# Performance work log

Hardware: AMD Instinct MI355X
Metric: run time of the kernel (lower is better)

Reference implementation:

```python
import jax, jax.numpy as jnp
import numpy as np

N = 100000    # nodes
E = 1200000   # edges (avg degree 12)
D0, D1 = 512, 256         # modality input dims
H, L, DEC = 500, 128, 64  # encoder hidden, latent, decoder dims
F1, F2, C = 64, 64, 8     # gnn hidden feats, num classes
EPS = 1e-5


def _bn(x, g, b, m, v):
    # inference-mode BatchNorm1d with running stats
    return (x - m) * jax.lax.rsqrt(v + EPS) * g + b


def _encoder(x, W1, b1, g1, be1, m1, v1, W2, b2, g2, be2, m2, v2, Wd, bd):
    e = _bn(x @ W1.T + b1, g1, be1, m1, v1)   # [N, H]
    e = _bn(e @ W2.T + b2, g2, be2, m2, v2)   # [N, L]
    return e @ Wd.T + bd                      # decoded: [N, DEC]


def _sage_pool(h, src, dst, Wp, bp, Ws, Wn, b):
    # DGL SAGEConv aggregator_type='pool' (feat_drop is identity in eval):
    # h_neigh[v] = max_{u in N(v)} relu(fc_pool(h[u])); out = fc_self(h) + fc_neigh(h_neigh) + bias
    m = jax.nn.relu(h @ Wp.T + bp)                              # [N, Din]
    agg = jax.ops.segment_max(m[src], dst, num_segments=N)      # gather + max-scatter
    agg = jnp.where(jnp.isfinite(agg), agg, 0.0)                # isolated nodes -> 0 (DGL)
    return h @ Ws.T + agg @ Wn.T + b


def setup_inputs() -> dict:
    key = jax.random.key(0)
    ks = iter(jax.random.split(key, 80))

    def nrm(sh, s=0.02):
        return jax.random.normal(next(ks), sh, jnp.float32) * s

    inp = {}
    inp["x0"] = jax.random.normal(next(ks), (N, D0), jnp.float32)
    inp["x1"] = jax.random.normal(next(ks), (N, D1), jnp.float32)
    inp["src"] = jax.random.randint(next(ks), (E,), 0, N, jnp.int32)
    inp["dst"] = jax.random.randint(next(ks), (E,), 0, N, jnp.int32)
    for mi, d in enumerate((D0, D1)):
        p = f"enc{mi}_"
        inp[p + "W1"] = nrm((H, d)); inp[p + "b1"] = jnp.zeros((H,), jnp.float32)
        inp[p + "g1"] = jnp.ones((H,), jnp.float32); inp[p + "be1"] = jnp.zeros((H,), jnp.float32)
        inp[p + "m1"] = nrm((H,), 0.1)
        inp[p + "v1"] = jax.random.uniform(next(ks), (H,), jnp.float32, 0.5, 1.5)
        inp[p + "W2"] = nrm((L, H)); inp[p + "b2"] = jnp.zeros((L,), jnp.float32)
        inp[p + "g2"] = jnp.ones((L,), jnp.float32); inp[p + "be2"] = jnp.zeros((L,), jnp.float32)
        inp[p + "m2"] = nrm((L,), 0.1)
        inp[p + "v2"] = jax.random.uniform(next(ks), (L,), jnp.float32, 0.5, 1.5)
        inp[p + "Wd"] = nrm((DEC, L)); inp[p + "bd"] = jnp.zeros((DEC,), jnp.float32)
    for li, (i, o) in enumerate(((DEC, F1), (F1, F2), (F2, C))):
        p = f"s{li}_"
        inp[p + "Wp"] = nrm((i, i)); inp[p + "bp"] = jnp.zeros((i,), jnp.float32)
        inp[p + "Ws"] = nrm((o, i)); inp[p + "Wn"] = nrm((o, i))
        inp[p + "b"] = jnp.zeros((o,), jnp.float32)
    return inp


def reference(x0, x1, src, dst,
              enc0_W1, enc0_b1, enc0_g1, enc0_be1, enc0_m1, enc0_v1,
              enc0_W2, enc0_b2, enc0_g2, enc0_be2, enc0_m2, enc0_v2, enc0_Wd, enc0_bd,
              enc1_W1, enc1_b1, enc1_g1, enc1_be1, enc1_m1, enc1_v1,
              enc1_W2, enc1_b2, enc1_g2, enc1_be2, enc1_m2, enc1_v2, enc1_Wd, enc1_bd,
              s0_Wp, s0_bp, s0_Ws, s0_Wn, s0_b,
              s1_Wp, s1_bp, s1_Ws, s1_Wn, s1_b,
              s2_Wp, s2_bp, s2_Ws, s2_Wn, s2_b):
    d0 = _encoder(x0, enc0_W1, enc0_b1, enc0_g1, enc0_be1, enc0_m1, enc0_v1,
                  enc0_W2, enc0_b2, enc0_g2, enc0_be2, enc0_m2, enc0_v2, enc0_Wd, enc0_bd)
    d1 = _encoder(x1, enc1_W1, enc1_b1, enc1_g1, enc1_be1, enc1_m1, enc1_v1,
                  enc1_W2, enc1_b2, enc1_g2, enc1_be2, enc1_m2, enc1_v2, enc1_Wd, enc1_bd)
    # mean over modalities (dropout = identity in eval; imputation/reindex = identity with full coverage)
    feat = (d0 + d1) * 0.5
    h = jax.nn.relu(_sage_pool(feat, src, dst, s0_Wp, s0_bp, s0_Ws, s0_Wn, s0_b))
    h = jax.nn.relu(_sage_pool(h, src, dst, s1_Wp, s1_bp, s1_Ws, s1_Wn, s1_b))
    h = _sage_pool(h, src, dst, s2_Wp, s2_bp, s2_Ws, s2_Wn, s2_b)  # [N, C]
    return h
```

## Files before the change

### kernel.cpp

```cpp
#include <hip/hip_runtime.h>
#include <hip/hip_bf16.h>

#define EPSV 1e-5f
#define NBUCK_C 400
using u16 = unsigned short;
using u32 = unsigned int;
typedef __attribute__((ext_vector_type(8))) short short8;
typedef __attribute__((ext_vector_type(4))) float f32x4;

__device__ __forceinline__ u16 f2bf(float f) {
  __hip_bfloat16 h = __float2bfloat16(f);
  u16 u; __builtin_memcpy(&u, &h, 2); return u;
}

__device__ __forceinline__ void gload16(const void* g, void* l) {
  __builtin_amdgcn_global_load_lds(
      (const __attribute__((address_space(1))) void*)g,
      (__attribute__((address_space(3))) void*)l, 16, 0, 0);
}

__device__ __forceinline__ u32 mx2(u32 a, u32 b) {
  u32 ah = a & 0xFFFF0000u, bh = b & 0xFFFF0000u;
  u32 al = a & 0x0000FFFFu, bl = b & 0x0000FFFFu;
  return (ah > bh ? ah : bh) | (al > bl ? al : bl);
}
__device__ __forceinline__ uint4 mx4(uint4 a, uint4 b) {
  return make_uint4(mx2(a.x, b.x), mx2(a.y, b.y), mx2(a.z, b.z), mx2(a.w, b.w));
}

struct EncR { float4 a[4]; short8 b[2]; };

__global__ __launch_bounds__(256) void enc_fused64(
    const float* __restrict__ x0, const float* __restrict__ x1,
    const u16* __restrict__ W0, const u16* __restrict__ W1,
    const float* __restrict__ beff0, const float* __restrict__ beff1,
    const u16* __restrict__ Wp, const float* __restrict__ bp,
    u16* __restrict__ out, u16* __restrict__ mout, int M) {
  __shared__ u16 sA[64 * 64];
  __shared__ u16 sB[64 * 64];
  const int tid = threadIdx.x;
  const int l = tid & 63;
  const int w = tid >> 6;
  const int row0 = blockIdx.x * 64;
  const int lc = l & 15;
  const int koff = (l >> 4) * 8;

  f32x4 acc[4];
#pragma unroll
  for (int nf = 0; nf < 4; ++nf) acc[nf] = f32x4{0.f, 0.f, 0.f, 0.f};

  auto loadstep = [&](EncR& rs, int s) {
    const int ph = s >= 8;
    const float* X = ph ? x1 : x0;
    const u16* W = ph ? W1 : W0;
    const int lda = ph ? 256 : 512;
    const int kb = (s - (ph ? 8 : 0)) * 64;
#pragma unroll
    for (int c = 0; c < 2; ++c) {
      const int r = c * 32 + (tid >> 3);
      const int gr = min(row0 + r, M - 1);
      const float* gp = &X[(size_t)gr * lda + kb + ((tid & 7) << 3)];
      rs.a[c * 2] = *(const float4*)gp;
      rs.a[c * 2 + 1] = *(const float4*)(gp + 4);
    }
#pragma unroll
    for (int i = 0; i < 2; ++i) {
      const int s2 = tid * 2 + i;
      const int rb = s2 >> 3, sl = s2 & 7;
      rs.b[i] = *(const short8*)&W[rb * lda + kb + sl * 8];
    }
  };
  auto storestep = [&](const EncR& rs) {
#pragma unroll
    for (int c = 0; c < 2; ++c) {
      const int r = c * 32 + (tid >> 3);
      const int ssl = tid & 7;
      short8 pk;
#pragma unroll
      for (int j = 0; j < 4; ++j) pk[j] = (short)f2bf(rs.a[c * 2][j]);
#pragma unroll
      for (int j = 0; j < 4; ++j) pk[4 + j] = (short)f2bf(rs.a[c * 2 + 1][j]);
      *(short8*)&sA[r * 64 + ((ssl ^ (r & 7)) << 3)] = pk;
    }
#pragma unroll
    for (int i = 0; i < 2; ++i) {
      const int s2 = tid * 2 + i;
      const int rb = s2 >> 3, sl = s2 & 7;
      *(short8*)&sB[rb * 64 + ((sl ^ (rb & 7)) << 3)] = rs.b[i];
    }
  };
  auto compute = [&]() {
#pragma unroll
    for (int kk = 0; kk < 2; ++kk) {
      const int r = w * 16 + lc;
      const int sl = kk * 4 + (l >> 4);
      const short8 af = *(const short8*)&sA[r * 64 + ((sl ^ (r & 7)) << 3)];
#pragma unroll
      for (int nf = 0; nf < 4; ++nf) {
        const int rb = nf * 16 + lc;
        const short8 bf = *(const short8*)&sB[rb * 64 + ((sl ^ (rb & 7)) << 3)];
        acc[nf] = __builtin_amdgcn_mfma_f32_16x16x32_bf16(af, bf, acc[nf], 0, 0, 0);
      }
    }
  };

  EncR rA, rB;
  loadstep(rA, 0);
  for (int s = 0; s < 12; s += 2) {
    loadstep(rB, s + 1);
    storestep(rA);
    __syncthreads();
    compute();
    __syncthreads();
    if (s + 2 < 12) loadstep(rA, s + 2);
    storestep(rB);
    __syncthreads();
    compute();
    __syncthreads();
  }

  const int lj = l >> 4;
#pragma unroll
  for (int nf = 0; nf < 4; ++nf) {
    const int col = nf * 16 + lc;
    const float sh = beff0[col] + beff1[col];
#pragma unroll
    for (int j = 0; j < 4; ++j) {
      const int r = w * 16 + lj * 4 + j;
      const u16 hv = f2bf(acc[nf][j] + sh);
      sA[r * 64 + ((((col >> 3) ^ (r & 7)) << 3) | (col & 7))] = hv;
      const int row = row0 + r;
      if (row < M) out[(size_t)row * 64 + col] = hv;
    }
  }
  __syncthreads();

  f32x4 acc2[4];
#pragma unroll
  for (int nf = 0; nf < 4; ++nf) acc2[nf] = f32x4{0.f, 0.f, 0.f, 0.f};
#pragma unroll
  for (int kk = 0; kk < 2; ++kk) {
    const int r = w * 16 + lc;
    const int sl = kk * 4 + (l >> 4);
    const short8 af = *(const short8*)&sA[r * 64 + ((sl ^ (r & 7)) << 3)];
#pragma unroll
    for (int nf = 0; nf < 4; ++nf) {
      const short8 bf =
          *(const short8*)&Wp[(size_t)(nf * 16 + lc) * 64 + kk * 32 + koff];
      acc2[nf] = __builtin_amdgcn_mfma_f32_16x16x32_bf16(af, bf, acc2[nf], 0, 0, 0);
    }
  }
#pragma unroll
  for (int nf = 0; nf < 4; ++nf) {
    const int col = nf * 16 + lc;
    const float sh = bp[col];
#pragma unroll
    for (int j = 0; j < 4; ++j) {
      const int row = row0 + w * 16 + lj * 4 + j;
      if (row < M)
        mout[(size_t)row * 64 + col] = f2bf(fmaxf(acc2[nf][j] + sh, 0.f));
    }
  }
}

__global__ __launch_bounds__(256) void sage_fused(
    const u16* __restrict__ A, const u16* __restrict__ A2,
    const u16* __restrict__ B, const u16* __restrict__ B2,
    const float* __restrict__ bias, const u16* __restrict__ Wp,
    const float* __restrict__ bp, u16* __restrict__ Hout,
    u16* __restrict__ Mout, int M) {
  __shared__ u16 sA[128 * 64];
  __shared__ u16 sB[64 * 64];
  __shared__ u16 sA2[128 * 64];
  __shared__ u16 sB2[64 * 64];
  const int tid = threadIdx.x;
  const int l = tid & 63;
  const int w = tid >> 6;
  const int wm = w >> 1, wn = w & 1;
  const int row0 = blockIdx.x * 128;
  const int lc = l & 15;
  const int koff = (l >> 4) * 8;
  const int srl = l >> 3, ssl = l & 7;

  f32x4 acc[4][2];
#pragma unroll
  for (int mf = 0; mf < 4; ++mf)
#pragma unroll
    for (int nf = 0; nf < 2; ++nf) acc[mf][nf] = f32x4{0.f, 0.f, 0.f, 0.f};

#pragma unroll
  for (int c = 0; c < 4; ++c) {
    const int r = c * 32 + w * 8 + srl;
    const int gr = min(row0 + r, M - 1);
    const int gk = (ssl ^ (r & 7)) << 3;
    gload16(&A[(size_t)gr * 64 + gk], &sA[(c * 32 + w * 8) * 64]);
    gload16(&A2[(size_t)gr * 64 + gk], &sA2[(c * 32 + w * 8) * 64]);
  }
#pragma unroll
  for (int c = 0; c < 2; ++c) {
    const int r = c * 32 + w * 8 + srl;
    const int gk = (ssl ^ (r & 7)) << 3;
    gload16(&B[(size_t)r * 64 + gk], &sB[(c * 32 + w * 8) * 64]);
    gload16(&B2[(size_t)r * 64 + gk], &sB2[(c * 32 + w * 8) * 64]);
  }
  __syncthreads();
#pragma unroll
  for (int kk = 0; kk < 2; ++kk) {
    short8 af[4], bfr[2], af2[4], bf2[2];
#pragma unroll
    for (int mf = 0; mf < 4; ++mf) {
      const int r = wm * 64 + mf * 16 + lc;
      const int sl = kk * 4 + (l >> 4);
      const int idx = r * 64 + ((sl ^ (r & 7)) << 3);
      af[mf] = *(const short8*)&sA[idx];
      af2[mf] = *(const short8*)&sA2[idx];
    }
#pragma unroll
    for (int nf = 0; nf < 2; ++nf) {
      const int r = wn * 32 + nf * 16 + lc;
      const int sl = kk * 4 + (l >> 4);
      const int idx = r * 64 + ((sl ^ (r & 7)) << 3);
      bfr[nf] = *(const short8*)&sB[idx];
      bf2[nf] = *(const short8*)&sB2[idx];
    }
#pragma unroll
    for (int mf = 0; mf < 4; ++mf)
#pragma unroll
      for (int nf = 0; nf < 2; ++nf) {
        acc[mf][nf] = __builtin_amdgcn_mfma_f32_16x16x32_bf16(
            af[mf], bfr[nf], acc[mf][nf], 0, 0, 0);
        acc[mf][nf] = __builtin_amdgcn_mfma_f32_16x16x32_bf16(
            af2[mf], bf2[nf], acc[mf][nf], 0, 0, 0);
      }
  }
  __syncthreads();

  const int lj = l >> 4;
#pragma unroll
  for (int mf = 0; mf < 4; ++mf)
#pragma unroll
    for (int nf = 0; nf < 2; ++nf) {
      const int col = wn * 32 + nf * 16 + lc;
      const float sh = bias[col];
#pragma unroll
      for (int j = 0; j < 4; ++j) {
        const int r = wm * 64 + mf * 16 + lj * 4 + j;
        const u16 hv = f2bf(fmaxf(acc[mf][nf][j] + sh, 0.f));
        sA[r * 64 + ((((col >> 3) ^ (r & 7)) << 3) | (col & 7))] = hv;
        const int row = row0 + r;
        if (row < M) Hout[(size_t)row * 64 + col] = hv;
      }
    }
  __syncthreads();

  f32x4 acc2[4][2];
#pragma unroll
  for (int mf = 0; mf < 4; ++mf)
#pragma unroll
    for (int nf = 0; nf < 2; ++nf) acc2[mf][nf] = f32x4{0.f, 0.f, 0.f, 0.f};
#pragma unroll
  for (int kk = 0; kk < 2; ++kk) {
    short8 af[4], bf[2];
#pragma unroll
    for (int mf = 0; mf < 4; ++mf) {
      const int r = wm * 64 + mf * 16 + lc;
      const int sl = kk * 4 + (l >> 4);
      af[mf] = *(const short8*)&sA[r * 64 + ((sl ^ (r & 7)) << 3)];
    }
#pragma unroll
    for (int nf = 0; nf < 2; ++nf)
      bf[nf] = *(const short8*)&Wp[(size_t)(wn * 32 + nf * 16 + lc) * 64 +
                                   kk * 32 + koff];
#pragma unroll
    for (int mf = 0; mf < 4; ++mf)
#pragma unroll
      for (int nf = 0; nf < 2; ++nf)
        acc2[mf][nf] = __builtin_amdgcn_mfma_f32_16x16x32_bf16(
            af[mf], bf[nf], acc2[mf][nf], 0, 0, 0);
  }
#pragma unroll
  for (int mf = 0; mf < 4; ++mf)
#pragma unroll
    for (int nf = 0; nf < 2; ++nf) {
      const int col = wn * 32 + nf * 16 + lc;
      const float sh = bp[col];
#pragma unroll
      for (int j = 0; j < 4; ++j) {
        const int row = row0 + wm * 64 + mf * 16 + lj * 4 + j;
        if (row < M)
          Mout[(size_t)row * 64 + col] = f2bf(fmaxf(acc2[mf][nf][j] + sh, 0.f));
      }
    }
}

template <int BN, int EPI, bool DUAL, bool AF32, bool BIAS2, typename OUT>
__global__ __launch_bounds__(256) void gemm_mfma(
    const void* __restrict__ A, int lda, const u16* __restrict__ B, int ldb,
    const u16* __restrict__ A2, const u16* __restrict__ B2, void* __restrict__ C,
    int ldc, int M, int Nout, int K, int storeN, int nby,
    const float* __restrict__ bias, const float* __restrict__ bnb,
    const float* __restrict__ bng, const float* __restrict__ bnbe,
    const float* __restrict__ bnm, const float* __restrict__ bnv) {
  constexpr int WN = BN / 2;
  constexpr int NF = WN / 16;
  constexpr int MF = 4;
  __shared__ u16 sA[128 * 64];
  __shared__ u16 sB[BN * 64];
  __shared__ u16 sA2[DUAL ? 128 * 64 : 8];
  __shared__ u16 sB2[DUAL ? BN * 64 : 8];

  const int nb = gridDim.x;
  const int orig = blockIdx.x;
  const int q = nb >> 3, rr = nb & 7;
  const int xcd = orig & 7, idx = orig >> 3;
  const int wg = (xcd < rr ? xcd * (q + 1) : rr * (q + 1) + (xcd - rr) * q) + idx;
  const int bx = wg / nby;
  const int by = wg % nby;

  const int tid = threadIdx.x;
  const int l = tid & 63;
  const int w = tid >> 6;
  const int wm = w >> 1, wn = w & 1;
  const int row0 = bx * 128;
  const int col0 = by * BN;

  f32x4 acc[MF][NF];
#pragma unroll
  for (int mf = 0; mf < MF; ++mf)
#pragma unroll
    for (int nf = 0; nf < NF; ++nf) acc[mf][nf] = f32x4{0.f, 0.f, 0.f, 0.f};

  const int srl = l >> 3;
  const int ssl = l & 7;
  const u16* Ab = (const u16*)A;
  const float* Af = (const float*)A;

  const int ksteps = K >> 6;
  for (int kt = 0; kt < ksteps; ++kt) {
    const int kb = kt * 64;
    if constexpr (AF32) {
      const int ssl2 = tid & 7;
#pragma unroll
      for (int c = 0; c < 4; ++c) {
        const int r = c * 32 + (tid >> 3);
        const int gr = min(row0 + r, M - 1);
        const float* gp = &Af[(size_t)gr * lda + kb + (ssl2 << 3)];
        float4 f0 = *(const float4*)gp;
        float4 f1 = *(const float4*)(gp + 4);
        short8 pk;
        pk[0] = (short)f2bf(f0.x); pk[1] = (short)f2bf(f0.y);
        pk[2] = (short)f2bf(f0.z); pk[3] = (short)f2bf(f0.w);
        pk[4] = (short)f2bf(f1.x); pk[5] = (short)f2bf(f1.y);
        pk[6] = (short)f2bf(f1.z); pk[7] = (short)f2bf(f1.w);
        *(short8*)&sA[r * 64 + ((ssl2 ^ (r & 7)) << 3)] = pk;
      }
    } else {
#pragma unroll
      for (int c = 0; c < 4; ++c) {
        const int r = c * 32 + w * 8 + srl;
        const int gr = min(row0 + r, M - 1);
        const int gk = kb + ((ssl ^ (r & 7)) << 3);
        gload16(&Ab[(size_t)gr * lda + gk], &sA[(c * 32 + w * 8) * 64]);
        if (DUAL) gload16(&A2[(size_t)gr * lda + gk], &sA2[(c * 32 + w * 8) * 64]);
      }
    }
#pragma unroll
    for (int c = 0; c < BN / 32; ++c) {
      const int r = c * 32 + w * 8 + srl;
      const int gr = min(col0 + r, Nout - 1);
      const int gk = kb + ((ssl ^ (r & 7)) << 3);
      gload16(&B[(size_t)gr * ldb + gk], &sB[(c * 32 + w * 8) * 64]);
      if (DUAL) gload16(&B2[(size_t)gr * ldb + gk], &sB2[(c * 32 + w * 8) * 64]);
    }
    __syncthreads();
#pragma unroll
    for (int kk = 0; kk < 2; ++kk) {
      short8 af[MF], bfr[NF], af2[MF], bf2[NF];
#pragma unroll
      for (int mf = 0; mf < MF; ++mf) {
        const int r = wm * 64 + mf * 16 + (l & 15);
        const int sl = kk * 4 + (l >> 4);
        const int idx2 = r * 64 + ((sl ^ (r & 7)) << 3);
        af[mf] = *(const short8*)&sA[idx2];
        if (DUAL) af2[mf] = *(const short8*)&sA2[idx2];
      }
#pragma unroll
      for (int nf = 0; nf < NF; ++nf) {
        const int r = wn * WN + nf * 16 + (l & 15);
        const int sl = kk * 4 + (l >> 4);
        const int idx2 = r * 64 + ((sl ^ (r & 7)) << 3);
        bfr[nf] = *(const short8*)&sB[idx2];
        if (DUAL) bf2[nf] = *(const short8*)&sB2[idx2];
      }
#pragma unroll
      for (int mf = 0; mf < MF; ++mf)
#pragma unroll
        for (int nf = 0; nf < NF; ++nf) {
          acc[mf][nf] = __builtin_amdgcn_mfma_f32_16x16x32_bf16(
              af[mf], bfr[nf], acc[mf][nf], 0, 0, 0);
          if (DUAL)
            acc[mf][nf] = __builtin_amdgcn_mfma_f32_16x16x32_bf16(
                af2[mf], bf2[nf], acc[mf][nf], 0, 0, 0);
        }
    }
    __syncthreads();
  }

  const int lj = l >> 4;
  const int lc = l & 15;
#pragma unroll
  for (int mf = 0; mf < MF; ++mf)
#pragma unroll
    for (int nf = 0; nf < NF; ++nf) {
      const int col = col0 + wn * WN + nf * 16 + lc;
      if (col >= storeN) continue;
      const bool cok = col < Nout;
      float sc = 0.f, sh = 0.f;
      if (cok) {
        if (EPI == 2) {
          sc = bng[col] * rsqrtf(bnv[col] + EPSV);
          sh = (bnb[col] - bnm[col]) * sc + bnbe[col];
        } else {
          sh = bias[col];
          if (BIAS2) sh += bnb[col];
        }
      }
#pragma unroll
      for (int j = 0; j < 4; ++j) {
        const int row = row0 + wm * 64 + mf * 16 + lj * 4 + j;
        if (row >= M) continue;
        float v = 0.f;
        if (cok) {
          v = acc[mf][nf][j];
          if (EPI == 2) v = v * sc + sh;
          else { v += sh; if (EPI == 1) v = fmaxf(v, 0.f); }
        }
        const size_t idx2 = (size_t)row * ldc + col;
        if constexpr (sizeof(OUT) == 2) ((u16*)C)[idx2] = f2bf(v);
        else ((float*)C)[idx2] = v;
      }
    }
}

struct WConv {
  const float* src[9];
  u16* dst[9];
  int n[9];
};
__global__ __launch_bounds__(256) void wconv_k(WConv wc) {
  const int t = blockIdx.y;
  const float* in = wc.src[t];
  u16* out = wc.dst[t];
  const int n = wc.n[t];
  const int stride4 = gridDim.x * blockDim.x * 4;
  for (int i4 = (blockIdx.x * blockDim.x + threadIdx.x) * 4; i4 < n; i4 += stride4) {
    float4 f = *(const float4*)&in[i4];
    ushort4 o;
    o.x = f2bf(f.x); o.y = f2bf(f.y); o.z = f2bf(f.z); o.w = f2bf(f.w);
    *(ushort4*)&out[i4] = o;
  }
}

__global__ __launch_bounds__(256) void combine_wcf(
    const float* __restrict__ W2, const float* __restrict__ b2,
    const float* __restrict__ g2, const float* __restrict__ be2,
    const float* __restrict__ m2, const float* __restrict__ v2,
    const float* __restrict__ Wd, const float* __restrict__ bd,
    float* __restrict__ Wcf, float* __restrict__ cc) {
  const int o = blockIdx.y;
  const int k = blockIdx.x * 256 + threadIdx.x;
  __shared__ float t2[128];
  if (threadIdx.x < 128) {
    const int j = threadIdx.x;
    const float s = g2[j] * rsqrtf(v2[j] + EPSV);
    t2[j] = Wd[o * 128 + j] * s;
  }
  __syncthreads();
  if (k < 500) {
    float accv = 0.f;
    for (int j = 0; j < 128; ++j) accv += t2[j] * W2[j * 500 + k];
    Wcf[o * 500 + k] = 0.5f * accv;
  }
  if (blockIdx.x == 0 && threadIdx.x == 0) {
    float accv = bd[o];
    for (int j = 0; j < 128; ++j) {
      const float s = g2[j] * rsqrtf(v2[j] + EPSV);
      accv += Wd[o * 128 + j] * ((b2[j] - m2[j]) * s + be2[j]);
    }
    cc[o] = 0.5f * accv;
  }
}

__global__ __launch_bounds__(256) void weff2_k(
    const float* __restrict__ Wcf, const float* __restrict__ cc,
    const float* __restrict__ g1, const float* __restrict__ be1,
    const float* __restrict__ b1, const float* __restrict__ m1,
    const float* __restrict__ v1, const float* __restrict__ W1, int D,
    u16* __restrict__ Weffb, float* __restrict__ beff) {
  const int o = blockIdx.y;
  const int t = threadIdx.x;
  __shared__ float wcs[500];
  __shared__ float psum[256];
  for (int j = t; j < 500; j += 256) {
    const float s = g1[j] * rsqrtf(v1[j] + EPSV);
    wcs[j] = Wcf[o * 500 + j] * s;
  }
  __syncthreads();
  const int dl = t & 63, jt = t >> 6;
  const int d = blockIdx.x * 64 + dl;
  const int j0 = jt * 125;
  float accv = 0.f;
  if (d < D) {
    for (int j = j0; j < j0 + 125; ++j) accv += wcs[j] * W1[(size_t)j * D + d];
  }
  psum[t] = accv;
  __syncthreads();
  if (jt == 0 && d < D) {
    const float tot = psum[dl] + psum[64 + dl] + psum[128 + dl] + psum[192 + dl];
    Weffb[o * D + d] = f2bf(tot);
  }
  if (blockIdx.x == 0) {
    __syncthreads();
    float pb = 0.f;
    for (int j = t; j < 500; j += 256) {
      const float s = g1[j] * rsqrtf(v1[j] + EPSV);
      pb += Wcf[o * 500 + j] * ((b1[j] - m1[j]) * s + be1[j]);
    }
    psum[t] = pb;
    __syncthreads();
    for (int off2 = 128; off2 > 0; off2 >>= 1) {
      if (t < off2) psum[t] += psum[t + off2];
      __syncthreads();
    }
    if (t == 0) beff[o] = psum[0] + cc[o];
  }
}

__global__ __launch_bounds__(256) void bhist_k(const int* __restrict__ dst,
                                               int* __restrict__ bhist, int ne,
                                               int nbuck, int epb) {
  __shared__ int cnt[NBUCK_C];
  const int t = threadIdx.x;
  for (int i = t; i < nbuck; i += 256) cnt[i] = 0;
  __syncthreads();
  const int e0 = blockIdx.x * epb;
  const int e1 = min(e0 + epb, ne);
  for (int i = e0 + t; i < e1; i += 256) atomicAdd(&cnt[dst[i] >> 8], 1);
  __syncthreads();
  for (int i = t; i < nbuck; i += 256) {
    const int c = cnt[i];
    if (c) atomicAdd(&bhist[i], c);
  }
}

__global__ __launch_bounds__(512) void bscan_k(const int* __restrict__ bhist,
                                               int* __restrict__ base,
                                               int* __restrict__ cursor,
                                               int nbuck, int ne) {
  __shared__ int lds[512];
  const int t = threadIdx.x;
  const int v = t < nbuck ? bhist[t] : 0;
  lds[t] = v;
  __syncthreads();
  for (int o = 1; o < 512; o <<= 1) {
    const int u = t >= o ? lds[t - o] : 0;
    __syncthreads();
    lds[t] += u;
    __syncthreads();
  }
  if (t < nbuck) {
    const int ex = lds[t] - v;
    base[t] = ex;
    cursor[t] = ex;
  }
  if (t == 0) base[nbuck] = ne;
}

__global__ __launch_bounds__(256) void bscat_k(const int* __restrict__ src,
                                               const int* __restrict__ dst,
                                               int* __restrict__ cursor,
                                               u32* __restrict__ tmp, int ne,
                                               int nbuck, int epb) {
  __shared__ int cnt[NBUCK_C];
  __shared__ int gbase[NBUCK_C];
  const int t = threadIdx.x;
  for (int i = t; i < nbuck; i += 256) cnt[i] = 0;
  __syncthreads();
  const int e0 = blockIdx.x * epb;
  const int e1 = min(e0 + epb, ne);
  for (int i = e0 + t; i < e1; i += 256) atomicAdd(&cnt[dst[i] >> 8], 1);
  __syncthreads();
  for (int i = t; i < nbuck; i += 256) {
    const int c = cnt[i];
    gbase[i] = c ? atomicAdd(&cursor[i], c) : 0;
    cnt[i] = 0;
  }
  __syncthreads();
  for (int i = e0 + t; i < e1; i += 256) {
    const int d = dst[i];
    const int b = d >> 8;
    const int p = atomicAdd(&cnt[b], 1);
    tmp[gbase[b] + p] = ((u32)src[i] << 8) | (u32)(d & 255);
  }
}

__global__ __launch_bounds__(256) void bsort_k(const u32* __restrict__ tmp,
                                               const int* __restrict__ base,
                                               int* __restrict__ rp,
                                               int* __restrict__ csr, int n) {
  const int b = blockIdx.x;
  const int t = threadIdx.x;
  __shared__ int cnt[256];
  __shared__ int loc[256];
  const int segbase = base[b];
  const int len = base[b + 1] - segbase;
  cnt[t] = 0;
  __syncthreads();
  for (int i = t; i < len; i += 256) atomicAdd(&cnt[tmp[segbase + i] & 255], 1);
  __syncthreads();
  const int own = cnt[t];
  __syncthreads();
  for (int o = 1; o < 256; o <<= 1) {
    const int u = t >= o ? cnt[t - o] : 0;
    __syncthreads();
    cnt[t] += u;
    __syncthreads();
  }
  const int pre = cnt[t] - own;
  loc[t] = pre;
  const int gnode = b * 256 + t;
  if (gnode <= n) rp[gnode] = segbase + pre;
  __syncthreads();
  for (int i = t; i < len; i += 256) {
    const u32 v = tmp[segbase + i];
    const int p = atomicAdd(&loc[v & 255], 1);
    csr[segbase + p] = (int)(v >> 8);
  }
}

__global__ __launch_bounds__(256) void gather_k(
    const u16* __restrict__ m, const int* __restrict__ csr,
    const int* __restrict__ rp, u16* __restrict__ agg, int n) {
  const int t = threadIdx.x;
  const int v = blockIdx.x * 32 + (t >> 3);
  if (v >= n) return;
  const int l = t & 7;
  const int base = rp[v];
  const int dg = rp[v + 1] - base;
  uint4 mx = make_uint4(0u, 0u, 0u, 0u);
  int i = 0;
  for (; i + 4 <= dg; i += 4) {
    const int u0 = csr[base + i + 0];
    const int u1 = csr[base + i + 1];
    const int u2 = csr[base + i + 2];
    const int u3 = csr[base + i + 3];
    const uint4 v0 = *(const uint4*)&m[(size_t)u0 * 64 + l * 8];
    const uint4 v1 = *(const uint4*)&m[(size_t)u1 * 64 + l * 8];
    const uint4 v2 = *(const uint4*)&m[(size_t)u2 * 64 + l * 8];
    const uint4 v3 = *(const uint4*)&m[(size_t)u3 * 64 + l * 8];
    mx = mx4(mx, mx4(mx4(v0, v1), mx4(v2, v3)));
  }
  for (; i < dg; ++i) {
    const int u = csr[base + i];
    const uint4 val = *(const uint4*)&m[(size_t)u * 64 + l * 8];
    mx = mx4(mx, val);
  }
  *(uint4*)&agg[(size_t)v * 64 + l * 8] = mx;
}

extern "C" void kernel_launch(void* const* d_in, const int* in_sizes, int n_in,
                              void* d_out, int out_size, void* d_ws,
                              size_t ws_size, hipStream_t stream) {
  const int N = 100000;
  const int NE = in_sizes[2];
  const float* x0 = (const float*)d_in[0];
  const float* x1 = (const float*)d_in[1];
  const int* src = (const int*)d_in[2];
  const int* dst = (const int*)d_in[3];
  auto F = [&](int i) { return (const float*)d_in[i]; };

  char* wsb = (char*)d_ws;
  size_t off = 0;
  auto alloc = [&](size_t bytes) {
    void* p = wsb + off;
    off += (bytes + 255) & ~(size_t)255;
    return p;
  };
  float* Wcf0 = (float*)alloc(64 * 500 * 4);
  float* Wcf1 = (float*)alloc(64 * 500 * 4);
  float* cc0 = (float*)alloc(64 * 4);
  float* cc1 = (float*)alloc(64 * 4);
  u16* Weff0b = (u16*)alloc(64 * 512 * 2);
  u16* Weff1b = (u16*)alloc(64 * 256 * 2);
  float* beff0 = (float*)alloc(64 * 4);
  float* beff1 = (float*)alloc(64 * 4);
  u16* swb[9];
  const int swsrc[9] = {32, 34, 35, 37, 39, 40, 42, 44, 45};
  const int swn[9] = {4096, 4096, 4096, 4096, 4096, 4096, 4096, 512, 512};
  for (int i = 0; i < 9; ++i) swb[i] = (u16*)alloc(swn[i] * 2);
  u16* featb = (u16*)alloc((size_t)N * 64 * 2);
  u16* mb = (u16*)alloc((size_t)N * 64 * 2);
  u16* aggb = (u16*)alloc((size_t)N * 64 * 2);
  u16* h1b = (u16*)alloc((size_t)N * 64 * 2);
  u16* h2b = (u16*)alloc((size_t)N * 64 * 2);
  const int NBUCK = (N + 255) / 256;
  int* rp = (int*)alloc((size_t)(N + 1) * 4);
  int* csr = (int*)alloc((size_t)NE * 4);
  u32* tmp = (u32*)alloc((size_t)NE * 4);
  int* bhist = (int*)alloc((size_t)NBUCK * 4);
  int* base = (int*)alloc((size_t)(NBUCK + 1) * 4);
  int* cursor = (int*)alloc((size_t)NBUCK * 4);
  (void)n_in; (void)ws_size;

  WConv wc;
  for (int i = 0; i < 9; ++i) {
    wc.src[i] = F(swsrc[i]); wc.dst[i] = swb[i]; wc.n[i] = swn[i];
  }
  wconv_k<<<dim3(8, 9), 256, 0, stream>>>(wc);
  combine_wcf<<<dim3(2, 64), 256, 0, stream>>>(F(10), F(11), F(12), F(13),
                                               F(14), F(15), F(16), F(17),
                                               Wcf0, cc0);
  combine_wcf<<<dim3(2, 64), 256, 0, stream>>>(F(24), F(25), F(26), F(27),
                                               F(28), F(29), F(30), F(31),
                                               Wcf1, cc1);
  weff2_k<<<dim3(8, 64), 256, 0, stream>>>(Wcf0, cc0, F(6), F(7), F(5), F(8),
                                           F(9), F(4), 512, Weff0b, beff0);
  weff2_k<<<dim3(4, 64), 256, 0, stream>>>(Wcf1, cc1, F(20), F(21), F(19),
                                           F(22), F(23), F(18), 256, Weff1b,
                                           beff1);

  const int NSB = 512;
  const int EPB = (NE + NSB - 1) / NSB;
  hipMemsetAsync(bhist, 0, (size_t)NBUCK * 4, stream);
  bhist_k<<<NSB, 256, 0, stream>>>(dst, bhist, NE, NBUCK, EPB);
  bscan_k<<<1, 512, 0, stream>>>(bhist, base, cursor, NBUCK, NE);
  bscat_k<<<NSB, 256, 0, stream>>>(src, dst, cursor, tmp, NE, NBUCK, EPB);
  bsort_k<<<NBUCK, 256, 0, stream>>>(tmp, base, rp, csr, N);

  enc_fused64<<<(N + 63) / 64, 256, 0, stream>>>(x0, x1, Weff0b, Weff1b,
                                                 beff0, beff1, swb[0], F(33),
                                                 featb, mb, N);

  const int gx = (N + 127) / 128;
  const int gg = (N + 31) / 32;
  gather_k<<<gg, 256, 0, stream>>>(mb, csr, rp, aggb, N);
  sage_fused<<<gx, 256, 0, stream>>>(featb, aggb, swb[1], swb[2], F(36),
                                     swb[3], F(38), h1b, mb, N);
  gather_k<<<gg, 256, 0, stream>>>(mb, csr, rp, aggb, N);
  sage_fused<<<gx, 256, 0, stream>>>(h1b, aggb, swb[4], swb[5], F(41),
                                     swb[6], F(43), h2b, mb, N);
  gather_k<<<gg, 256, 0, stream>>>(mb, csr, rp, aggb, N);
  gemm_mfma<64, 0, true, false, false, float><<<gx, 256, 0, stream>>>(
      h2b, 64, swb[7], 64, aggb, swb[8], d_out, 8, N, 8, 64, 8, 1, F(46),
      nullptr, nullptr, nullptr, nullptr, nullptr);
  (void)out_size;
}
```

Before: 340.7 us.

## Fuse neighbor max-gather into SAGE GEMM kernels, eliminating aggregate buffer

The separate gather_k kernel that wrote the neighbor max-aggregate to global memory is removed. Each SAGE layer kernel (and a new final-layer kernel) now computes the CSR max-gather for its 128-row tile straight into shared memory before the MFMA GEMM. Ping-pong message buffers replace the single buffer so a layer can read the previous messages while writing new ones. This removes the aggregate write and re-read plus three launches, but puts the irregular gather latency inside the GEMM blocks, where it may be harder to hide at lower occupancy.

```diff
diff --git a/kernel.cpp b/kernel.cpp
--- a/kernel.cpp
+++ b/kernel.cpp
@@ -26,6 +26,29 @@
 }
 __device__ __forceinline__ uint4 mx4(uint4 a, uint4 b) {
   return make_uint4(mx2(a.x, b.x), mx2(a.y, b.y), mx2(a.z, b.z), mx2(a.w, b.w));
+}
+
+__device__ __forceinline__ uint4 gather_row(const u16* __restrict__ m,
+                                            const int* __restrict__ csr,
+                                            int base, int dg, int gl) {
+  uint4 mx = make_uint4(0u, 0u, 0u, 0u);
+  int i = 0;
+  for (; i + 4 <= dg; i += 4) {
+    const int u0 = csr[base + i + 0];
+    const int u1 = csr[base + i + 1];
+    const int u2 = csr[base + i + 2];
+    const int u3 = csr[base + i + 3];
+    const uint4 v0 = *(const uint4*)&m[(size_t)u0 * 64 + gl * 8];
+    const uint4 v1 = *(const uint4*)&m[(size_t)u1 * 64 + gl * 8];
+    const uint4 v2 = *(const uint4*)&m[(size_t)u2 * 64 + gl * 8];
+    const uint4 v3 = *(const uint4*)&m[(size_t)u3 * 64 + gl * 8];
+    mx = mx4(mx, mx4(mx4(v0, v1), mx4(v2, v3)));
+  }
+  for (; i < dg; ++i) {
+    const int u = csr[base + i];
+    mx = mx4(mx, *(const uint4*)&m[(size_t)u * 64 + gl * 8]);
+  }
+  return mx;
 }
 
 struct EncR { float4 a[4]; short8 b[2]; };
@@ -163,8 +186,9 @@
   }
 }
 
-__global__ __launch_bounds__(256) void sage_fused(
-    const u16* __restrict__ A, const u16* __restrict__ A2,
+__global__ __launch_bounds__(256) void sage_g_fused(
+    const u16* __restrict__ A, const u16* __restrict__ magg,
+    const int* __restrict__ csr, const int* __restrict__ rp,
     const u16* __restrict__ B, const u16* __restrict__ B2,
     const float* __restrict__ bias, const u16* __restrict__ Wp,
     const float* __restrict__ bp, u16* __restrict__ Hout,
@@ -182,19 +206,12 @@
   const int koff = (l >> 4) * 8;
   const int srl = l >> 3, ssl = l & 7;
 
-  f32x4 acc[4][2];
-#pragma unroll
-  for (int mf = 0; mf < 4; ++mf)
-#pragma unroll
-    for (int nf = 0; nf < 2; ++nf) acc[mf][nf] = f32x4{0.f, 0.f, 0.f, 0.f};
-
 #pragma unroll
   for (int c = 0; c < 4; ++c) {
     const int r = c * 32 + w * 8 + srl;
     const int gr = min(row0 + r, M - 1);
     const int gk = (ssl ^ (r & 7)) << 3;
     gload16(&A[(size_t)gr * 64 + gk], &sA[(c * 32 + w * 8) * 64]);
-    gload16(&A2[(size_t)gr * 64 + gk], &sA2[(c * 32 + w * 8) * 64]);
   }
 #pragma unroll
   for (int c = 0; c < 2; ++c) {
@@ -203,7 +220,29 @@
     gload16(&B[(size_t)r * 64 + gk], &sB[(c * 32 + w * 8) * 64]);
     gload16(&B2[(size_t)r * 64 + gk], &sB2[(c * 32 + w * 8) * 64]);
   }
-  __syncthreads();
+  {
+    const int gl = tid & 7;
+    const int gn = tid >> 3;
+#pragma unroll
+    for (int p = 0; p < 4; ++p) {
+      const int r = p * 32 + gn;
+      const int v = row0 + r;
+      uint4 mx = make_uint4(0u, 0u, 0u, 0u);
+      if (v < M) {
+        const int base = rp[v];
+        const int dg = rp[v + 1] - base;
+        mx = gather_row(magg, csr, base, dg, gl);
+      }
+      *(uint4*)&sA2[r * 64 + ((gl ^ (r & 7)) << 3)] = mx;
+    }
+  }
+  __syncthreads();
+
+  f32x4 acc[4][2];
+#pragma unroll
+  for (int mf = 0; mf < 4; ++mf)
+#pragma unroll
+    for (int nf = 0; nf < 2; ++nf) acc[mf][nf] = f32x4{0.f, 0.f, 0.f, 0.f};
 #pragma unroll
   for (int kk = 0; kk < 2; ++kk) {
     short8 af[4], bfr[2], af2[4], bf2[2];
@@ -293,151 +332,103 @@
     }
 }
 
-template <int BN, int EPI, bool DUAL, bool AF32, bool BIAS2, typename OUT>
-__global__ __launch_bounds__(256) void gemm_mfma(
-    const void* __restrict__ A, int lda, const u16* __restrict__ B, int ldb,
-    const u16* __restrict__ A2, const u16* __restrict__ B2, void* __restrict__ C,
-    int ldc, int M, int Nout, int K, int storeN, int nby,
-    const float* __restrict__ bias, const float* __restrict__ bnb,
-    const float* __restrict__ bng, const float* __restrict__ bnbe,
-    const float* __restrict__ bnm, const float* __restrict__ bnv) {
-  constexpr int WN = BN / 2;
-  constexpr int NF = WN / 16;
-  constexpr int MF = 4;
+__global__ __launch_bounds__(256) void final_g(
+    const u16* __restrict__ A, const u16* __restrict__ magg,
+    const int* __restrict__ csr, const int* __restrict__ rp,
+    const u16* __restrict__ B, const u16* __restrict__ B2,
+    const float* __restrict__ bias, float* __restrict__ C, int M) {
   __shared__ u16 sA[128 * 64];
-  __shared__ u16 sB[BN * 64];
-  __shared__ u16 sA2[DUAL ? 128 * 64 : 8];
-  __shared__ u16 sB2[DUAL ? BN * 64 : 8];
-
-  const int nb = gridDim.x;
-  const int orig = blockIdx.x;
-  const int q = nb >> 3, rr = nb & 7;
-  const int xcd = orig & 7, idx = orig >> 3;
-  const int wg = (xcd < rr ? xcd * (q + 1) : rr * (q + 1) + (xcd - rr) * q) + idx;
-  const int bx = wg / nby;
-  const int by = wg % nby;
-
+  __shared__ u16 sB[64 * 64];
+  __shared__ u16 sA2[128 * 64];
+  __shared__ u16 sB2[64 * 64];
   const int tid = threadIdx.x;
   const int l = tid & 63;
   const int w = tid >> 6;
   const int wm = w >> 1, wn = w & 1;
-  const int row0 = bx * 128;
-  const int col0 = by * BN;
-
-  f32x4 acc[MF][NF];
-#pragma unroll
-  for (int mf = 0; mf < MF; ++mf)
-#pragma unroll
-    for (int nf = 0; nf < NF; ++nf) acc[mf][nf] = f32x4{0.f, 0.f, 0.f, 0.f};
-
-  const int srl = l >> 3;
-  const int ssl = l & 7;
-  const u16* Ab = (const u16*)A;
-  const float* Af = (const float*)A;
-
-  const int ksteps = K >> 6;
-  for (int kt = 0; kt < ksteps; ++kt) {
-    const int kb = kt * 64;
-    if constexpr (AF32) {
-      const int ssl2 = tid & 7;
-#pragma unroll
-      for (int c = 0; c < 4; ++c) {
-        const int r = c * 32 + (tid >> 3);
-        const int gr = min(row0 + r, M - 1);
-        const float* gp = &Af[(size_t)gr * lda + kb + (ssl2 << 3)];
-        float4 f0 = *(const float4*)gp;
-        float4 f1 = *(const float4*)(gp + 4);
-        short8 pk;
-        pk[0] = (short)f2bf(f0.x); pk[1] = (short)f2bf(f0.y);
-        pk[2] = (short)f2bf(f0.z); pk[3] = (short)f2bf(f0.w);
-        pk[4] = (short)f2bf(f1.x); pk[5] = (short)f2bf(f1.y);
-        pk[6] = (short)f2bf(f1.z); pk[7] = (short)f2bf(f1.w);
-        *(short8*)&sA[r * 64 + ((ssl2 ^ (r & 7)) << 3)] = pk;
+  const int row0 = blockIdx.x * 128;
+  const int lc = l & 15;
+  const int srl = l >> 3, ssl = l & 7;
+
+#pragma unroll
+  for (int c = 0; c < 4; ++c) {
+    const int r = c * 32 + w * 8 + srl;
+    const int gr = min(row0 + r, M - 1);
+    const int gk = (ssl ^ (r & 7)) << 3;
+    gload16(&A[(size_t)gr * 64 + gk], &sA[(c * 32 + w * 8) * 64]);
+  }
+#pragma unroll
+  for (int c = 0; c < 2; ++c) {
+    const int r = c * 32 + w * 8 + srl;
+    const int gr = min(r, 7);
+    const int gk = (ssl ^ (r & 7)) << 3;
+    gload16(&B[(size_t)gr * 64 + gk], &sB[(c * 32 + w * 8) * 64]);
+    gload16(&B2[(size_t)gr * 64 + gk], &sB2[(c * 32 + w * 8) * 64]);
+  }
+  {
+    const int gl = tid & 7;
+    const int gn = tid >> 3;
+#pragma unroll
+    for (int p = 0; p < 4; ++p) {
+      const int r = p * 32 + gn;
+      const int v = row0 + r;
+      uint4 mx = make_uint4(0u, 0u, 0u, 0u);
+      if (v < M) {
+        const int base = rp[v];
+        const int dg = rp[v + 1] - base;
+        mx = gather_row(magg, csr, base, dg, gl);
       }
-    } else {
-#pragma unroll
-      for (int c = 0; c < 4; ++c) {
-        const int r = c * 32 + w * 8 + srl;
-        const int gr = min(row0 + r, M - 1);
-        const int gk = kb + ((ssl ^ (r & 7)) << 3);
-        gload16(&Ab[(size_t)gr * lda + gk], &sA[(c * 32 + w * 8) * 64]);
-        if (DUAL) gload16(&A2[(size_t)gr * lda + gk], &sA2[(c * 32 + w * 8) * 64]);
+      *(uint4*)&sA2[r * 64 + ((gl ^ (r & 7)) << 3)] = mx;
+    }
+  }
+  __syncthreads();
+
+  f32x4 acc[4][2];
+#pragma unroll
+  for (int mf = 0; mf < 4; ++mf)
+#pragma unroll
+    for (int nf = 0; nf < 2; ++nf) acc[mf][nf] = f32x4{0.f, 0.f, 0.f, 0.f};
+#pragma unroll
+  for (int kk = 0; kk < 2; ++kk) {
+    short8 af[4], bfr[2], af2[4], bf2[2];
+#pragma unroll
+    for (int mf = 0; mf < 4; ++mf) {
+      const int r = wm * 64 + mf * 16 + lc;
+      const int sl = kk * 4 + (l >> 4);
+      const int idx = r * 64 + ((sl ^ (r & 7)) << 3);
+      af[mf] = *(const short8*)&sA[idx];
+      af2[mf] = *(const short8*)&sA2[idx];
+    }
+#pragma unroll
+    for (int nf = 0; nf < 2; ++nf) {
+      const int r = wn * 32 + nf * 16 + lc;
+      const int sl = kk * 4 + (l >> 4);
+      const int idx = r * 64 + ((sl ^ (r & 7)) << 3);
+      bfr[nf] = *(const short8*)&sB[idx];
+      bf2[nf] = *(const short8*)&sB2[idx];
+    }
+#pragma unroll
+    for (int mf = 0; mf < 4; ++mf)
+#pragma unroll
+      for (int nf = 0; nf < 2; ++nf) {
+        acc[mf][nf] = __builtin_amdgcn_mfma_f32_16x16x32_bf16(
+            af[mf], bfr[nf], acc[mf][nf], 0, 0, 0);
+        acc[mf][nf] = __builtin_amdgcn_mfma_f32_16x16x32_bf16(
+            af2[mf], bf2[nf], acc[mf][nf], 0, 0, 0);
       }
-    }
-#pragma unroll
-    for (int c = 0; c < BN / 32; ++c) {
-      const int r = c * 32 + w * 8 + srl;
-      const int gr = min(col0 + r, Nout - 1);
-      const int gk = kb + ((ssl ^ (r & 7)) << 3);
-      gload16(&B[(size_t)gr * ldb + gk], &sB[(c * 32 + w * 8) * 64]);
-      if (DUAL) gload16(&B2[(size_t)gr * ldb + gk], &sB2[(c * 32 + w * 8) * 64]);
-    }
-    __syncthreads();
-#pragma unroll
-    for (int kk = 0; kk < 2; ++kk) {
-      short8 af[MF], bfr[NF], af2[MF], bf2[NF];
-#pragma unroll
-      for (int mf = 0; mf < MF; ++mf) {
-        const int r = wm * 64 + mf * 16 + (l & 15);
-        const int sl = kk * 4 + (l >> 4);
-        const int idx2 = r * 64 + ((sl ^ (r & 7)) << 3);
-        af[mf] = *(const short8*)&sA[idx2];
-        if (DUAL) af2[mf] = *(const short8*)&sA2[idx2];
-      }
-#pragma unroll
-      for (int nf = 0; nf < NF; ++nf) {
-        const int r = wn * WN + nf * 16 + (l & 15);
-        const int sl = kk * 4 + (l >> 4);
-        const int idx2 = r * 64 + ((sl ^ (r & 7)) << 3);
-        bfr[nf] = *(const short8*)&sB[idx2];
-        if (DUAL) bf2[nf] = *(const short8*)&sB2[idx2];
-      }
-#pragma unroll
-      for (int mf = 0; mf < MF; ++mf)
-#pragma unroll
-        for (int nf = 0; nf < NF; ++nf) {
-          acc[mf][nf] = __builtin_amdgcn_mfma_f32_16x16x32_bf16(
-              af[mf], bfr[nf], acc[mf][nf], 0, 0, 0);
-          if (DUAL)
-            acc[mf][nf] = __builtin_amdgcn_mfma_f32_16x16x32_bf16(
-                af2[mf], bf2[nf], acc[mf][nf], 0, 0, 0);
-        }
-    }
-    __syncthreads();
   }
 
   const int lj = l >> 4;
-  const int lc = l & 15;
-#pragma unroll
-  for (int mf = 0; mf < MF; ++mf)
-#pragma unroll
-    for (int nf = 0; nf < NF; ++nf) {
-      const int col = col0 + wn * WN + nf * 16 + lc;
-      if (col >= storeN) continue;
-      const bool cok = col < Nout;
-      float sc = 0.f, sh = 0.f;
-      if (cok) {
-        if (EPI == 2) {
-          sc = bng[col] * rsqrtf(bnv[col] + EPSV);
-          sh = (bnb[col] - bnm[col]) * sc + bnbe[col];
-        } else {
-          sh = bias[col];
-          if (BIAS2) sh += bnb[col];
-        }
-      }
+#pragma unroll
+  for (int mf = 0; mf < 4; ++mf)
+#pragma unroll
+    for (int nf = 0; nf < 2; ++nf) {
+      const int col = wn * 32 + nf * 16 + lc;
+      if (col >= 8) continue;
+      const float sh = bias[col];
 #pragma unroll
       for (int j = 0; j < 4; ++j) {
         const int row = row0 + wm * 64 + mf * 16 + lj * 4 + j;
-        if (row >= M) continue;
-        float v = 0.f;
-        if (cok) {
-          v = acc[mf][nf][j];
-          if (EPI == 2) v = v * sc + sh;
-          else { v += sh; if (EPI == 1) v = fmaxf(v, 0.f); }
-        }
-        const size_t idx2 = (size_t)row * ldc + col;
-        if constexpr (sizeof(OUT) == 2) ((u16*)C)[idx2] = f2bf(v);
-        else ((float*)C)[idx2] = v;
+        if (row < M) C[(size_t)row * 8 + col] = acc[mf][nf][j] + sh;
       }
     }
 }
@@ -636,36 +627,6 @@
     const int p = atomicAdd(&loc[v & 255], 1);
     csr[segbase + p] = (int)(v >> 8);
   }
-}
-
-__global__ __launch_bounds__(256) void gather_k(
-    const u16* __restrict__ m, const int* __restrict__ csr,
-    const int* __restrict__ rp, u16* __restrict__ agg, int n) {
-  const int t = threadIdx.x;
-  const int v = blockIdx.x * 32 + (t >> 3);
-  if (v >= n) return;
-  const int l = t & 7;
-  const int base = rp[v];
-  const int dg = rp[v + 1] - base;
-  uint4 mx = make_uint4(0u, 0u, 0u, 0u);
-  int i = 0;
-  for (; i + 4 <= dg; i += 4) {
-    const int u0 = csr[base + i + 0];
-    const int u1 = csr[base + i + 1];
-    const int u2 = csr[base + i + 2];
-    const int u3 = csr[base + i + 3];
-    const uint4 v0 = *(const uint4*)&m[(size_t)u0 * 64 + l * 8];
-    const uint4 v1 = *(const uint4*)&m[(size_t)u1 * 64 + l * 8];
-    const uint4 v2 = *(const uint4*)&m[(size_t)u2 * 64 + l * 8];
-    const uint4 v3 = *(const uint4*)&m[(size_t)u3 * 64 + l * 8];
-    mx = mx4(mx, mx4(mx4(v0, v1), mx4(v2, v3)));
-  }
-  for (; i < dg; ++i) {
-    const int u = csr[base + i];
-    const uint4 val = *(const uint4*)&m[(size_t)u * 64 + l * 8];
-    mx = mx4(mx, val);
-  }
-  *(uint4*)&agg[(size_t)v * 64 + l * 8] = mx;
 }
 
 extern "C" void kernel_launch(void* const* d_in, const int* in_sizes, int n_in,
@@ -699,8 +660,8 @@
   const int swn[9] = {4096, 4096, 4096, 4096, 4096, 4096, 4096, 512, 512};
   for (int i = 0; i < 9; ++i) swb[i] = (u16*)alloc(swn[i] * 2);
   u16* featb = (u16*)alloc((size_t)N * 64 * 2);
-  u16* mb = (u16*)alloc((size_t)N * 64 * 2);
-  u16* aggb = (u16*)alloc((size_t)N * 64 * 2);
+  u16* mb0 = (u16*)alloc((size_t)N * 64 * 2);
+  u16* mb1 = (u16*)alloc((size_t)N * 64 * 2);
   u16* h1b = (u16*)alloc((size_t)N * 64 * 2);
   u16* h2b = (u16*)alloc((size_t)N * 64 * 2);
   const int NBUCK = (N + 255) / 256;
@@ -739,19 +700,14 @@
 
   enc_fused64<<<(N + 63) / 64, 256, 0, stream>>>(x0, x1, Weff0b, Weff1b,
                                                  beff0, beff1, swb[0], F(33),
-                                                 featb, mb, N);
+                                                 featb, mb0, N);
 
   const int gx = (N + 127) / 128;
-  const int gg = (N + 31) / 32;
-  gather_k<<<gg, 256, 0, stream>>>(mb, csr, rp, aggb, N);
-  sage_fused<<<gx, 256, 0, stream>>>(featb, aggb, swb[1], swb[2], F(36),
-                                     swb[3], F(38), h1b, mb, N);
-  gather_k<<<gg, 256, 0, stream>>>(mb, csr, rp, aggb, N);
-  sage_fused<<<gx, 256, 0, stream>>>(h1b, aggb, swb[4], swb[5], F(41),
-                                     swb[6], F(43), h2b, mb, N);
-  gather_k<<<gg, 256, 0, stream>>>(mb, csr, rp, aggb, N);
-  gemm_mfma<64, 0, true, false, false, float><<<gx, 256, 0, stream>>>(
-      h2b, 64, swb[7], 64, aggb, swb[8], d_out, 8, N, 8, 64, 8, 1, F(46),
-      nullptr, nullptr, nullptr, nullptr, nullptr);
+  sage_g_fused<<<gx, 256, 0, stream>>>(featb, mb0, csr, rp, swb[1], swb[2],
+                                       F(36), swb[3], F(38), h1b, mb1, N);
+  sage_g_fused<<<gx, 256, 0, stream>>>(h1b, mb1, csr, rp, swb[4], swb[5],
+                                       F(41), swb[6], F(43), h2b, mb0, N);
+  final_g<<<gx, 256, 0, stream>>>(h2b, mb0, csr, rp, swb[7], swb[8], F(46),
+                                  (float*)d_out, N);
   (void)out_size;
 }
```

New measurement: 387.8 us. +13.8%, slower.
